# Optimization experiments

Measured on AMD Instinct MI355X. Metric: run time of the kernel, lower is better.

## Reference

```python
import jax, jax.numpy as jnp
import numpy as np

B, N, C, H, W = 8, 512, 3, 16, 16
K, P, E = 2, 4, 1           # K: hop levels == filter taps, P: attn heads, E: edge feature sets
SLOPE = 0.2                 # LeakyReLU slope in attention
GAT_DIMS = {'d0': (128, 128), 'd1': (512, 32), 'u0': (128, 64),
            'u1': (256, 128), 's0': (128, 128), 's1': (512, 64)}


def _conv(x, w, b):
    pad = w.shape[-1] // 2
    y = jax.lax.conv_general_dilated(x, w, (1, 1), [(pad, pad), (pad, pad)],
                                     dimension_numbers=('NCHW', 'OIHW', 'NCHW'))
    return y + b[None, :, None, None]


def _gat(x, S, wk, wq, wf, b):
    # x: (B,G,N); S: (B,E,N,N) binary GSO. KeyQuery attention + K-tap attentional filter.
    key = jnp.einsum('pegf,bgn->bpefn', wk, x)
    qry = jnp.einsum('pegf,bgn->bpefn', wq, x)
    # scores[...,n,m]: logit of node n attending to neighbor m
    scores = jax.nn.leaky_relu(jnp.einsum('bpefn,bpefm->bpenm', qry, key), SLOPE)
    mask = (jnp.abs(S) > 1e-9)[:, None]                    # (B,1,E,N,N)
    aij = jnp.where(mask, jax.nn.softmax(jnp.where(mask, scores, -1e9), axis=-1), 0.0)
    Pn, En, Kt, G, F = wf.shape
    xk = jnp.broadcast_to(x[:, None, None], (x.shape[0], Pn, En, G, x.shape[-1]))
    zs = [xk]
    for _ in range(Kt - 1):
        xk = jnp.einsum('bpegm,bpenm->bpegn', xk, aij)     # attention-weighted diffusion
        zs.append(xk)
    z = jnp.stack(zs, axis=3)                              # (B,P,E,K,G,N)
    y = jnp.einsum('bpekgn,pekgf->bpfn', z, wf) + b[None, None, :, None]
    y = jax.nn.relu(y)                                     # nonlinearity before head concat
    return y.reshape(y.shape[0], Pn * F, y.shape[-1])      # (B, P*F, N)


def _forward(x, Slist, conv0_w, conv0_b, conv1_w, conv1_b, flat_w, flat_b,
             d0_wk, d0_wq, d0_wf, d0_b, d1_wk, d1_wq, d1_wf, d1_b,
             u0_wk, u0_wq, u0_wf, u0_b, u1_wk, u1_wq, u1_wf, u1_b,
             s0_wk, s0_wq, s0_wf, s0_b, s1_wk, s1_wq, s1_wf, s1_b,
             dec0_w, dec0_b, dec1_w, dec1_b):
    Bn, Nn = x.shape[0], x.shape[1]
    h = x.reshape(Bn * Nn, C, H, W)
    e = jax.nn.relu(_conv(h, conv0_w, conv0_b))
    e = jax.nn.relu(_conv(e, conv1_w, conv1_b))
    e = e + h                                              # RES connection after encoder
    f = jax.nn.relu(e.reshape(Bn * Nn, -1) @ flat_w.T + flat_b)
    g = f.reshape(Bn, -1, Nn)                              # faithful torch reshape to (B, F, N)
    S0, S1 = Slist[:, 0:1], Slist[:, 1:2]
    p0 = g
    p1 = _gat(p0, S0, d0_wk, d0_wq, d0_wf, d0_b)           # downward pass
    p2 = _gat(p1, S1, d1_wk, d1_wq, d1_wf, d1_b)
    # upward pass + shortcuts (upward[l] uses S[K-l-1]; shortcut[K-1-l] on p[K-1-l])
    u0 = _gat(p2, S1, u0_wk, u0_wq, u0_wf, u0_b) + _gat(p1, S1, s1_wk, s1_wq, s1_wf, s1_b)
    u1 = _gat(u0, S0, u1_wk, u1_wq, u1_wf, u1_b) + _gat(p0, S0, s0_wk, s0_wq, s0_wf, s0_b)
    d = jax.nn.relu(u1.reshape(Bn * Nn, -1) @ dec0_w.T + dec0_b)
    out = jax.nn.softmax(d @ dec1_w.T + dec1_b, axis=-1)   # nn.Softmax() -> dim=1 on 2D input
    return out.reshape(Bn, Nn, -1)


def setup_inputs() -> dict:
    key = jax.random.key(0)
    ks = iter(jax.random.split(key, 64))
    def nrm(shape, s=0.1):
        return jax.random.normal(next(ks), shape, jnp.float32) * s
    x = jax.random.normal(next(ks), (B, N, C, H, W), jnp.float32)
    adj = (jax.random.uniform(next(ks), (B, K, N, N)) < 0.02).astype(jnp.float32)
    Slist = jnp.clip(adj + jnp.eye(N, dtype=jnp.float32)[None, None], 0.0, 1.0)
    inp = {'x': x, 'Slist': Slist,
           'conv0_w': nrm((32, C, 3, 3)), 'conv0_b': nrm((32,)),
           'conv1_w': nrm((C, 32, 3, 3)), 'conv1_b': nrm((C,)),
           'flat_w': nrm((128, C * H * W)), 'flat_b': nrm((128,))}
    for pre, (G, F) in GAT_DIMS.items():
        inp[pre + '_wk'] = nrm((P, E, G, F))
        inp[pre + '_wq'] = nrm((P, E, G, F))
        inp[pre + '_wf'] = nrm((P, E, K, G, F))
        inp[pre + '_b'] = nrm((F,))
    inp.update({'dec0_w': nrm((256, 512)), 'dec0_b': nrm((256,)),
                'dec1_w': nrm((5, 256)), 'dec1_b': nrm((5,))})
    return inp


def reference(x, Slist, conv0_w, conv0_b, conv1_w, conv1_b, flat_w, flat_b,
              d0_wk, d0_wq, d0_wf, d0_b, d1_wk, d1_wq, d1_wf, d1_b,
              u0_wk, u0_wq, u0_wf, u0_b, u1_wk, u1_wq, u1_wf, u1_b,
              s0_wk, s0_wq, s0_wf, s0_b, s1_wk, s1_wq, s1_wf, s1_b,
              dec0_w, dec0_b, dec1_w, dec1_b):
    return _forward(x, Slist, conv0_w, conv0_b, conv1_w, conv1_b, flat_w, flat_b,
                    d0_wk, d0_wq, d0_wf, d0_b, d1_wk, d1_wq, d1_wf, d1_b,
                    u0_wk, u0_wq, u0_wf, u0_b, u1_wk, u1_wq, u1_wf, u1_b,
                    s0_wk, s0_wq, s0_wf, s0_b, s1_wk, s1_wq, s1_wf, s1_b,
                    dec0_w, dec0_b, dec1_w, dec1_b)
```

## Files before the change

### kernel.cpp

```cpp
#include <hip/hip_runtime.h>
#include <hip/hip_bf16.h>
#include <math.h>

typedef unsigned short u16;
typedef unsigned int   u32;
typedef unsigned long long u64;

#define CAP 48

__device__ __forceinline__ float tof(u16 u){
  union { u32 i; float f; } v; v.i = ((u32)u) << 16; return v.f;
}
__device__ __forceinline__ u16 fromf(float f){
  union { float f; u32 i; } v; v.f = f;
  u32 x = v.i;
  return (u16)((x + 0x7fffu + ((x >> 16) & 1u)) >> 16);
}

__global__ void detect_dtype(const void* xp, int* flag){
  if(threadIdx.x == 0 && blockIdx.x == 0){
    const u16* p = (const u16*)xp;
    int outl = 0;
    for(int i = 0; i < 128; i++){
      u16 u = p[2*i];
      int e = (u >> 7) & 0xFF;
      if(u != 0 && (e < 100 || e > 140)) outl++;
    }
    *flag = (outl > 32) ? 1 : 0;
  }
}

struct WArgs {
  const void* p[34];
  int sz[34];
  int off[35];
};

__global__ __launch_bounds__(256) void convert_weights(WArgs wa, const int* flag,
                                                       float* __restrict__ arena, int total){
  int i = blockIdx.x * 256 + threadIdx.x;
  if(i >= total) return;
  int isf = *flag;
  int t = 0;
  while(wa.off[t+1] <= i) t++;
  int j = i - wa.off[t];
  float v = 0.f;
  if(j < wa.sz[t])
    v = isf ? ((const float*)wa.p[t])[j] : tof(((const u16*)wa.p[t])[j]);
  arena[i] = v;
}

__global__ __launch_bounds__(256) void transpose_w(const float* __restrict__ src,
                                                   float* __restrict__ dst, int R, int C){
  int i = blockIdx.x * 256 + threadIdx.x;
  if(i < R*C){
    int r = i / C, c = i - r*C;
    dst[(size_t)c*R + r] = src[i];
  }
}

__global__ __launch_bounds__(64) void build_nbr(const void* __restrict__ S,
                                                int* __restrict__ nbr_idx,
                                                int* __restrict__ nbr_cnt,
                                                const int* __restrict__ flag){
  int isf = *flag;
  int row  = blockIdx.x;
  int lane = threadIdx.x;
  int cnt = 0;
  for(int c = 0; c < 8; c++){
    int m = c*64 + lane;
    size_t idx = (size_t)row * 512 + m;
    float sv = isf ? ((const float*)S)[idx] : tof(((const u16*)S)[idx]);
    bool pred = fabsf(sv) > 1e-9f;
    unsigned long long mask = __ballot(pred);
    int pos = cnt + __popcll(mask & ((1ull << lane) - 1ull));
    if(pred && pos < CAP) nbr_idx[(size_t)row*CAP + pos] = m;
    cnt += __popcll(mask);
  }
  if(lane == 0) nbr_cnt[row] = cnt > CAP ? CAP : cnt;
}

__global__ __launch_bounds__(256) void encoder_conv(
    const void* __restrict__ x, const int* __restrict__ flag,
    const float* __restrict__ w0, const float* __restrict__ b0,
    const float* __restrict__ w1, const float* __restrict__ b1,
    float* __restrict__ e1n)
{
  __shared__ float xpad[3][18][18];
  __shared__ float e0p[16][18][18];

  int isf = *flag;
  int tid = threadIdx.x;
  size_t img = blockIdx.x;
  int py = tid >> 4, px = tid & 15;

  float* z1 = &xpad[0][0][0];
  for(int i = tid; i < 972; i += 256) z1[i] = 0.f;
  float* z2 = &e0p[0][0][0];
  for(int i = tid; i < 5184; i += 256) z2[i] = 0.f;
  __syncthreads();

  #pragma unroll
  for(int i = 0; i < 3; i++){
    size_t gi = img*768 + i*256 + tid;
    xpad[i][1+py][1+px] = isf ? ((const float*)x)[gi] : tof(((const u16*)x)[gi]);
  }
  __syncthreads();

  float acc1[3] = {0.f, 0.f, 0.f};

  for(int grp = 0; grp < 2; grp++){
    float acc0[16];
    #pragma unroll
    for(int o = 0; o < 16; o++) acc0[o] = 0.f;
    for(int i = 0; i < 3; i++){
      float rr[9];
      #pragma unroll
      for(int ky = 0; ky < 3; ky++)
        #pragma unroll
        for(int kx = 0; kx < 3; kx++)
          rr[ky*3+kx] = xpad[i][py+ky][px+kx];
      #pragma unroll
      for(int o = 0; o < 16; o++){
        #pragma unroll
        for(int t = 0; t < 9; t++)
          acc0[o] = fmaf(rr[t], w0[(grp*16+o)*27 + i*9 + t], acc0[o]);
      }
    }
    __syncthreads();
    #pragma unroll
    for(int o = 0; o < 16; o++)
      e0p[o][1+py][1+px] = fmaxf(acc0[o] + b0[grp*16 + o], 0.f);
    __syncthreads();

    for(int i = 0; i < 16; i++){
      float rr[9];
      #pragma unroll
      for(int ky = 0; ky < 3; ky++)
        #pragma unroll
        for(int kx = 0; kx < 3; kx++)
          rr[ky*3+kx] = e0p[i][py+ky][px+kx];
      int ic = grp*16 + i;
      #pragma unroll
      for(int o = 0; o < 3; o++){
        #pragma unroll
        for(int t = 0; t < 9; t++)
          acc1[o] = fmaf(rr[t], w1[o*288 + ic*9 + t], acc1[o]);
      }
    }
  }

  #pragma unroll
  for(int o = 0; o < 3; o++)
    e1n[img*768 + o*256 + tid] = fmaxf(acc1[o] + b1[o], 0.f) + xpad[o][1+py][1+px];
}

__global__ __launch_bounds__(256) void gemm_flat(
    const float* __restrict__ e1n, const float* __restrict__ fwT,
    const float* __restrict__ fb, float* __restrict__ g)
{
  __shared__ float As[16][68];
  __shared__ float Bs[16][68];
  int tid = threadIdx.x;
  int n0 = blockIdx.x * 64, m0 = blockIdx.y * 64;

  int lk = tid >> 4;
  int l4 = (tid & 15) * 4;
  int br = tid >> 2;
  int bc = (tid & 3) * 4;

  float acc[4][4];
  #pragma unroll
  for(int i = 0; i < 4; i++)
    #pragma unroll
    for(int jj = 0; jj < 4; jj++) acc[i][jj] = 0.f;

  int tm = tid >> 4, tn = tid & 15;
  for(int kt = 0; kt < 48; kt++){
    int k0 = kt*16;
    *(float4*)&As[lk][l4] = *(const float4*)&fwT[(size_t)(k0 + lk)*128 + m0 + l4];
    float4 bv = *(const float4*)&e1n[(size_t)(n0 + br)*768 + k0 + bc];
    Bs[bc+0][br] = bv.x; Bs[bc+1][br] = bv.y; Bs[bc+2][br] = bv.z; Bs[bc+3][br] = bv.w;
    __syncthreads();
    #pragma unroll
    for(int kk = 0; kk < 16; kk++){
      float4 a  = *(const float4*)&As[kk][tm*4];
      float4 xx = *(const float4*)&Bs[kk][tn*4];
      float av[4]  = {a.x, a.y, a.z, a.w};
      float xvv[4] = {xx.x, xx.y, xx.z, xx.w};
      #pragma unroll
      for(int i = 0; i < 4; i++)
        #pragma unroll
        for(int jj = 0; jj < 4; jj++)
          acc[i][jj] = fmaf(av[i], xvv[jj], acc[i][jj]);
    }
    __syncthreads();
  }

  #pragma unroll
  for(int jj = 0; jj < 4; jj++){
    int img = n0 + tn*4 + jj;
    float4 r = make_float4(fmaxf(acc[0][jj] + fb[m0+tm*4+0], 0.f),
                           fmaxf(acc[1][jj] + fb[m0+tm*4+1], 0.f),
                           fmaxf(acc[2][jj] + fb[m0+tm*4+2], 0.f),
                           fmaxf(acc[3][jj] + fb[m0+tm*4+3], 0.f));
    *(float4*)&g[(size_t)img*128 + m0 + tm*4] = r;
  }
}

struct KqP { const float* X; const float* wk; const float* wq; float* kqT;
             int G, F, my; };

__global__ __launch_bounds__(256) void gemm_kq2(KqP A, KqP B)
{
  __shared__ float Ws[32*68];
  __shared__ float Xs[32*68];
  int tid = threadIdx.x;
  int by = blockIdx.y;
  KqP P = (by < A.my) ? A : B;
  int lby = (by < A.my) ? by : (by - A.my);
  int bp = blockIdx.z;
  int b = bp >> 2, p = bp & 3;
  int n0 = blockIdx.x * 64, m0 = lby * 64;
  const float* Xb = P.X + (size_t)b * P.G * 512;

  int lk = tid >> 4;
  int l4 = (tid & 15) * 4;

  int mg = m0 + l4;
  int quad = mg / P.F;
  int mq = mg - quad * P.F;
  size_t GF = (size_t)P.G * P.F;
  const float* wb = (quad == 0 ? P.wk : P.wq) + (size_t)p * GF + mq;

  float acc[4][4];
  #pragma unroll
  for(int i = 0; i < 4; i++)
    #pragma unroll
    for(int jj = 0; jj < 4; jj++) acc[i][jj] = 0.f;

  int tm = tid >> 4, tn = tid & 15;
  int KT = P.G / 32;
  for(int kt = 0; kt < KT; kt++){
    int k = kt*32 + lk;
    *(float4*)&Ws[lk*68 + l4]      = *(const float4*)(wb + (size_t)k * P.F);
    *(float4*)&Ws[(lk+16)*68 + l4] = *(const float4*)(wb + (size_t)(k+16) * P.F);
    *(float4*)&Xs[lk*68 + l4]      = *(const float4*)(Xb + (size_t)k * 512 + n0 + l4);
    *(float4*)&Xs[(lk+16)*68 + l4] = *(const float4*)(Xb + (size_t)(k+16) * 512 + n0 + l4);
    __syncthreads();
    #pragma unroll
    for(int kk = 0; kk < 32; kk++){
      float4 a  = *(const float4*)&Ws[kk*68 + tm*4];
      float4 xx = *(const float4*)&Xs[kk*68 + tn*4];
      float av[4]  = {a.x, a.y, a.z, a.w};
      float xvv[4] = {xx.x, xx.y, xx.z, xx.w};
      #pragma unroll
      for(int i = 0; i < 4; i++)
        #pragma unroll
        for(int jj = 0; jj < 4; jj++)
          acc[i][jj] = fmaf(av[i], xvv[jj], acc[i][jj]);
    }
    __syncthreads();
  }

  int F2 = 2*P.F;
  float* ob = P.kqT + (size_t)bp * 512 * F2;
  #pragma unroll
  for(int jj = 0; jj < 4; jj++){
    float* orow = ob + (size_t)(n0 + tn*4 + jj) * F2 + m0 + tm*4;
    #pragma unroll
    for(int i = 0; i < 4; i++) orow[i] = acc[i][jj];
  }
}

struct AtP { const float* kqT; u64* ctrl; int F, s; };

__global__ __launch_bounds__(256) void attn2(
    AtP A, AtP B,
    const int* __restrict__ nbr_idx, const int* __restrict__ nbr_cnt)
{
  __shared__ float qs[16][132];
  __shared__ float sc[16][CAP];
  __shared__ float red[16][2];
  int tid = threadIdx.x;
  int n0 = blockIdx.x * 16;
  int bp = blockIdx.y;
  AtP P = (blockIdx.z == 0) ? A : B;
  int b = bp >> 2;
  int F = P.F;
  int F2 = 2*F;
  const float* kqT = P.kqT;

  int F4 = F >> 2;
  for(int i = tid; i < 16*F4; i += 256){
    int r = i / F4, c4 = (i - r*F4) * 4;
    *(float4*)&qs[r][c4] =
      *(const float4*)&kqT[((size_t)bp*512 + n0 + r)*F2 + F + c4];
  }
  __syncthreads();

  int r = tid >> 4;
  int t = tid & 15;
  int n = n0 + r;
  int srow = (b*2 + P.s)*512 + n;
  int cnt = nbr_cnt[srow];
  const int* il = nbr_idx + (size_t)srow * CAP;

  for(int j = t; j < cnt; j += 16){
    int m = il[j];
    const float* krow = kqT + ((size_t)bp*512 + m)*F2;
    float a = 0.f;
    for(int f = 0; f < F; f += 4){
      float4 k4 = *(const float4*)&krow[f];
      a = fmaf(qs[r][f],   k4.x, a);
      a = fmaf(qs[r][f+1], k4.y, a);
      a = fmaf(qs[r][f+2], k4.z, a);
      a = fmaf(qs[r][f+3], k4.w, a);
    }
    sc[r][j] = a >= 0.f ? a : 0.2f * a;
  }
  __syncthreads();

  if(t == 0){
    float mx = -1e30f;
    for(int j = 0; j < cnt; j++) mx = fmaxf(mx, sc[r][j]);
    float ssum = 0.f;
    for(int j = 0; j < cnt; j++) ssum += expf(sc[r][j] - mx);
    red[r][0] = mx; red[r][1] = ssum;
  }
  __syncthreads();

  float mx = red[r][0], ssum = red[r][1];
  u64* crow = P.ctrl + ((size_t)bp*512 + n)*CAP;
  for(int j = t; j < cnt; j += 16){
    float w = expf(sc[r][j] - mx) / ssum;
    crow[j] = (u64)__float_as_uint(w) | ((u64)(u32)il[j] << 32);
  }
}

struct FiP { const float* X; const u64* ctrl; float* Xp; int G, s, gy; };

__global__ __launch_bounds__(256) void fill_Xp4(
    FiP A, FiP B, const int* __restrict__ nbr_cnt)
{
  __shared__ float xi[512*18];

  int tid = threadIdx.x;
  int by = blockIdx.y;
  FiP P = (by < A.gy) ? A : B;
  int lby = (by < A.gy) ? by : (by - A.gy);
  int n0 = blockIdx.x * 64;
  int g0 = lby * 16;
  int bp = blockIdx.z;
  int b = bp >> 2;
  int srow0 = (b*2 + P.s)*512 + n0;

  const float* Xb = P.X + ((size_t)b * P.G + g0) * 512;
  for(int i = tid; i < 16*512; i += 256){
    int gl = i >> 9, m = i & 511;
    xi[m*18 + gl] = Xb[(size_t)gl*512 + m];
  }

  int n_l = tid & 63;
  int q   = tid >> 6;
  int cnt = nbr_cnt[srow0 + n_l];
  const u64* cn = P.ctrl + ((size_t)bp*512 + n0 + n_l)*CAP;
  __syncthreads();

  const float* xq = &xi[4*q];
  float a0=0.f, a1=0.f, a2=0.f, a3=0.f;
  for(int j0 = 0; j0 < cnt; j0 += 4){
    u64 c0 = cn[j0], c1 = cn[j0+1], c2 = cn[j0+2], c3 = cn[j0+3];
    int m0 = (int)(c0 >> 32) & 511;
    int m1 = (int)(c1 >> 32) & 511;
    int m2 = (int)(c2 >> 32) & 511;
    int m3 = (int)(c3 >> 32) & 511;
    float w0 = __uint_as_float((u32)c0);
    float w1 = (j0+1 < cnt) ? __uint_as_float((u32)c1) : 0.f;
    float w2 = (j0+2 < cnt) ? __uint_as_float((u32)c2) : 0.f;
    float w3 = (j0+3 < cnt) ? __uint_as_float((u32)c3) : 0.f;
    float2 g0a = *(const float2*)&xq[m0*18], g0b = *(const float2*)&xq[m0*18 + 2];
    float2 g1a = *(const float2*)&xq[m1*18], g1b = *(const float2*)&xq[m1*18 + 2];
    float2 g2a = *(const float2*)&xq[m2*18], g2b = *(const float2*)&xq[m2*18 + 2];
    float2 g3a = *(const float2*)&xq[m3*18], g3b = *(const float2*)&xq[m3*18 + 2];
    a0 = fmaf(w0, g0a.x, a0); a1 = fmaf(w0, g0a.y, a1);
    a2 = fmaf(w0, g0b.x, a2); a3 = fmaf(w0, g0b.y, a3);
    a0 = fmaf(w1, g1a.x, a0); a1 = fmaf(w1, g1a.y, a1);
    a2 = fmaf(w1, g1b.x, a2); a3 = fmaf(w1, g1b.y, a3);
    a0 = fmaf(w2, g2a.x, a0); a1 = fmaf(w2, g2a.y, a1);
    a2 = fmaf(w2, g2b.x, a2); a3 = fmaf(w2, g2b.y, a3);
    a0 = fmaf(w3, g3a.x, a0); a1 = fmaf(w3, g3a.y, a1);
    a2 = fmaf(w3, g3b.x, a2); a3 = fmaf(w3, g3b.y, a3);
  }

  float* ob = P.Xp + ((size_t)bp * P.G + g0 + 4*q) * 512 + n0 + n_l;
  ob[0]    = a0;
  ob[512]  = a1;
  ob[1024] = a2;
  ob[1536] = a3;
}

struct YP { const float* X; const float* Xp; const float* wf; const float* bias;
            float* out; int G, F, PF, acc, my; };

__global__ __launch_bounds__(256) void gemm_y2_32(YP A, YP B)
{
  __shared__ float Ws[32*68];
  __shared__ float Xs[32*68];
  int tid = threadIdx.x;
  int by = blockIdx.y;
  YP P = (by < A.my) ? A : B;
  int lby = (by < A.my) ? by : (by - A.my);
  int bp = blockIdx.z;
  int b = bp >> 2, p = bp & 3;
  int n0 = blockIdx.x * 64, m0 = lby * 64;
  int G = P.G, F = P.F;

  int lk = tid >> 4;
  int l4 = (tid & 15) * 4;
  int mg = m0 + l4;
  int fcl = mg < F ? mg : (F - 4);
  size_t GF2 = (size_t)2 * G * F;
  const float* wb = P.wf + (size_t)p * GF2 + fcl;

  float acc[4][4];
  #pragma unroll
  for(int i = 0; i < 4; i++)
    #pragma unroll
    for(int jj = 0; jj < 4; jj++) acc[i][jj] = 0.f;

  int tm = tid >> 4, tn = tid & 15;
  int KT = (2*G) / 32;
  for(int kt = 0; kt < KT; kt++){
    int c0 = kt*32 + lk;
    int c1 = c0 + 16;
    const float* xr0 = (c0 < G) ? (P.X  + ((size_t)b  * G + c0      ) * 512)
                                : (P.Xp + ((size_t)bp * G + (c0 - G)) * 512);
    const float* xr1 = (c1 < G) ? (P.X  + ((size_t)b  * G + c1      ) * 512)
                                : (P.Xp + ((size_t)bp * G + (c1 - G)) * 512);
    *(float4*)&Ws[lk*68 + l4]      = *(const float4*)(wb + (size_t)c0 * F);
    *(float4*)&Ws[(lk+16)*68 + l4] = *(const float4*)(wb + (size_t)c1 * F);
    *(float4*)&Xs[lk*68 + l4]      = *(const float4*)(xr0 + n0 + l4);
    *(float4*)&Xs[(lk+16)*68 + l4] = *(const float4*)(xr1 + n0 + l4);
    __syncthreads();
    #pragma unroll
    for(int kk = 0; kk < 32; kk++){
      float4 a  = *(const float4*)&Ws[kk*68 + tm*4];
      float4 xx = *(const float4*)&Xs[kk*68 + tn*4];
      float av[4]  = {a.x, a.y, a.z, a.w};
      float xvv[4] = {xx.x, xx.y, xx.z, xx.w};
      #pragma unroll
      for(int i = 0; i < 4; i++)
        #pragma unroll
        for(int jj = 0; jj < 4; jj++)
          acc[i][jj] = fmaf(av[i], xvv[jj], acc[i][jj]);
    }
    __syncthreads();
  }

  int mrow = m0 + tm*4;
  if(mrow < F){
    float* ob = P.out + ((size_t)b * P.PF + (size_t)p * F + mrow) * 512 + n0 + tn*4;
    #pragma unroll
    for(int i = 0; i < 4; i++){
      float bv = P.bias[mrow + i];
      float4 r = make_float4(fmaxf(acc[i][0] + bv, 0.f),
                             fmaxf(acc[i][1] + bv, 0.f),
                             fmaxf(acc[i][2] + bv, 0.f),
                             fmaxf(acc[i][3] + bv, 0.f));
      float* dst = ob + (size_t)i * 512;
      if(P.acc){
        float4 old = *(float4*)dst;
        r.x += old.x; r.y += old.y; r.z += old.z; r.w += old.w;
      }
      *(float4*)dst = r;
    }
  }
}

__global__ __launch_bounds__(256) void gemm_y2_K64(YP A, YP B)
{
  __shared__ float Ws[64*68];
  __shared__ float Xs[64*68];
  int tid = threadIdx.x;
  int by = blockIdx.y;
  YP P = (by < A.my) ? A : B;
  int lby = (by < A.my) ? by : (by - A.my);
  int bp = blockIdx.z;
  int b = bp >> 2, p = bp & 3;
  int n0 = blockIdx.x * 64, m0 = lby * 64;
  int G = P.G, F = P.F;

  int lk = tid >> 4;
  int l4 = (tid & 15) * 4;
  int mg = m0 + l4;
  int fcl = mg < F ? mg : (F - 4);
  size_t GF2 = (size_t)2 * G * F;
  const float* wb = P.wf + (size_t)p * GF2 + fcl;

  float acc[4][4];
  #pragma unroll
  for(int i = 0; i < 4; i++)
    #pragma unroll
    for(int jj = 0; jj < 4; jj++) acc[i][jj] = 0.f;

  int tm = tid >> 4, tn = tid & 15;
  int KT = (2*G) / 64;
  for(int kt = 0; kt < KT; kt++){
    #pragma unroll
    for(int kb = 0; kb < 4; kb++){
      int c = kt*64 + lk + kb*16;
      const float* xr = (c < G) ? (P.X  + ((size_t)b  * G + c      ) * 512)
                                : (P.Xp + ((size_t)bp * G + (c - G)) * 512);
      *(float4*)&Ws[(lk + kb*16)*68 + l4] = *(const float4*)(wb + (size_t)c * F);
      *(float4*)&Xs[(lk + kb*16)*68 + l4] = *(const float4*)(xr + n0 + l4);
    }
    __syncthreads();
    #pragma unroll
    for(int kk = 0; kk < 64; kk++){
      float4 a  = *(const float4*)&Ws[kk*68 + tm*4];
      float4 xx = *(const float4*)&Xs[kk*68 + tn*4];
      float av[4]  = {a.x, a.y, a.z, a.w};
      float xvv[4] = {xx.x, xx.y, xx.z, xx.w};
      #pragma unroll
      for(int i = 0; i < 4; i++)
        #pragma unroll
        for(int jj = 0; jj < 4; jj++)
          acc[i][jj] = fmaf(av[i], xvv[jj], acc[i][jj]);
    }
    __syncthreads();
  }

  int mrow = m0 + tm*4;
  if(mrow < F){
    float* ob = P.out + ((size_t)b * P.PF + (size_t)p * F + mrow) * 512 + n0 + tn*4;
    #pragma unroll
    for(int i = 0; i < 4; i++){
      float bv = P.bias[mrow + i];
      float4 r = make_float4(fmaxf(acc[i][0] + bv, 0.f),
                             fmaxf(acc[i][1] + bv, 0.f),
                             fmaxf(acc[i][2] + bv, 0.f),
                             fmaxf(acc[i][3] + bv, 0.f));
      float* dst = ob + (size_t)i * 512;
      if(P.acc){
        float4 old = *(float4*)dst;
        r.x += old.x; r.y += old.y; r.z += old.z; r.w += old.w;
      }
      *(float4*)dst = r;
    }
  }
}

__global__ __launch_bounds__(256) void add_vec(float* __restrict__ dst,
                                               const float* __restrict__ src, int n4){
  int i = blockIdx.x * 256 + threadIdx.x;
  if(i < n4){
    float4 a = ((const float4*)dst)[i];
    float4 b = ((const float4*)src)[i];
    a.x += b.x; a.y += b.y; a.z += b.z; a.w += b.w;
    ((float4*)dst)[i] = a;
  }
}

__global__ __launch_bounds__(256) void gemm_dec0(
    const float* __restrict__ u1, const float* __restrict__ w0T,
    const float* __restrict__ b0, float* __restrict__ d)
{
  __shared__ float As[16][68];
  __shared__ float Bs[16][68];
  int tid = threadIdx.x;
  int n0 = blockIdx.x * 64;
  int m0 = blockIdx.y * 64;

  int lk = tid >> 4;
  int l4 = (tid & 15) * 4;
  int br = tid >> 2;
  int bc = (tid & 3) * 4;

  float acc[4][4];
  #pragma unroll
  for(int i = 0; i < 4; i++)
    #pragma unroll
    for(int jj = 0; jj < 4; jj++) acc[i][jj] = 0.f;

  int tm = tid >> 4, tn = tid & 15;
  for(int kt = 0; kt < 32; kt++){
    int k0 = kt*16;
    *(float4*)&As[lk][l4] = *(const float4*)&w0T[(size_t)(k0 + lk)*256 + m0 + l4];
    float4 bv = *(const float4*)&u1[(size_t)(n0 + br)*512 + k0 + bc];
    Bs[bc+0][br] = bv.x; Bs[bc+1][br] = bv.y; Bs[bc+2][br] = bv.z; Bs[bc+3][br] = bv.w;
    __syncthreads();
    #pragma unroll
    for(int kk = 0; kk < 16; kk++){
      float4 a  = *(const float4*)&As[kk][tm*4];
      float4 xx = *(const float4*)&Bs[kk][tn*4];
      float av[4]  = {a.x, a.y, a.z, a.w};
      float xvv[4] = {xx.x, xx.y, xx.z, xx.w};
      #pragma unroll
      for(int i = 0; i < 4; i++)
        #pragma unroll
        for(int jj = 0; jj < 4; jj++)
          acc[i][jj] = fmaf(av[i], xvv[jj], acc[i][jj]);
    }
    __syncthreads();
  }

  #pragma unroll
  for(int jj = 0; jj < 4; jj++){
    int row = n0 + tn*4 + jj;
    float4 r = make_float4(fmaxf(acc[0][jj] + b0[m0+tm*4+0], 0.f),
                           fmaxf(acc[1][jj] + b0[m0+tm*4+1], 0.f),
                           fmaxf(acc[2][jj] + b0[m0+tm*4+2], 0.f),
                           fmaxf(acc[3][jj] + b0[m0+tm*4+3], 0.f));
    *(float4*)&d[(size_t)row*256 + m0 + tm*4] = r;
  }
}

__global__ __launch_bounds__(64) void decoder2(
    const float* __restrict__ d,
    const float* __restrict__ w1, const float* __restrict__ b1,
    const int* __restrict__ flag, void* __restrict__ outp)
{
  __shared__ float ds[256];
  __shared__ float lg[5];
  int r = blockIdx.x, lane = threadIdx.x;
  for(int i = lane; i < 256; i += 64) ds[i] = d[(size_t)r*256 + i];
  __syncthreads();

  if(lane < 5){
    float a = 0.f;
    const float* wr = w1 + (size_t)lane * 256;
    for(int i = 0; i < 256; i++) a = fmaf(ds[i], wr[i], a);
    lg[lane] = a + b1[lane];
  }
  __syncthreads();
  if(lane < 5){
    float mx = lg[0];
    for(int i = 1; i < 5; i++) mx = fmaxf(mx, lg[i]);
    float ssum = 0.f;
    for(int i = 0; i < 5; i++) ssum += expf(lg[i] - mx);
    float v = expf(lg[lane] - mx) / ssum;
    if(*flag) ((float*)outp)[(size_t)r*5 + lane] = v;
    else      ((u16*)outp)[(size_t)r*5 + lane] = fromf(v);
  }
}

extern "C" void kernel_launch(void* const* d_in, const int* in_sizes, int n_in,
                              void* d_out, int out_size, void* d_ws, size_t ws_size,
                              hipStream_t stream)
{
  (void)n_in; (void)out_size; (void)ws_size;
  const void* x = d_in[0];
  const void* S = d_in[1];

  float* wsf   = (float*)d_ws;
  int*   flag  = (int*)d_ws;
  float* arena = wsf + 1024;

  WArgs wa;
  long long aoff[35]; aoff[0] = 0;
  for(int t = 0; t < 34; t++){
    wa.p[t]  = d_in[2 + t];
    wa.sz[t] = in_sizes[2 + t];
    wa.off[t] = (int)aoff[t];
    aoff[t+1] = aoff[t] + ((in_sizes[2 + t] + 15) & ~15);
  }
  wa.off[34] = (int)aoff[34];
  int total = (int)aoff[34];

  size_t cur = 1024 + (size_t)((total + 1023) & ~1023);
  float* g    = wsf + cur; cur += 524288;
  float* p1   = wsf + cur; cur += 2097152;
  float* p2   = wsf + cur; cur += 524288;
  float* u0b  = wsf + cur; cur += 1048576;
  float* u0c  = wsf + cur; cur += 1048576;
  float* u1c  = wsf + cur; cur += 2097152;
  float* u1b  = p1;
  u64*   ctrlA= (u64*)(wsf + cur); cur += (size_t)32*512*CAP*2;
  u64*   ctrlB= (u64*)(wsf + cur); cur += (size_t)32*512*CAP*2;
  float* fwT  = wsf + cur; cur += 98304;
  float* dw0T = wsf + cur; cur += 131072;
  int*   ncnt = (int*)(wsf + cur); cur += 8192;
  int*   nidx = (int*)(wsf + cur); cur += (size_t)8192 * CAP;
  float* pool = wsf + cur; cur += 10485760;

  float* e1n   = pool;
  float* kqT0  = pool;
  float* Xp0   = pool;
  float* kqT1  = pool;
  float* kqT5  = pool + 4194304;
  float* Xp1   = pool;
  float* Xp5   = pool + 8388608;
  float* kqT2  = pool;
  float* kqT3  = pool + 2097152;
  float* Xp2   = pool;
  float* Xp3   = pool + 2097152;
  float* kqT4  = pool;
  float* Xp4   = pool;
  float* dbuf  = pool;

  const float* A[34];
  for(int t = 0; t < 34; t++) A[t] = arena + aoff[t];
  const float* c0w = A[0], *c0b = A[1], *c1w = A[2], *c1b = A[3];
  const float* fw  = A[4], *fb  = A[5];
  const float *wk_[6], *wq_[6], *wf_[6], *bias_[6];
  for(int l = 0; l < 6; l++){
    wk_[l]   = A[6 + 4*l];
    wq_[l]   = A[7 + 4*l];
    wf_[l]   = A[8 + 4*l];
    bias_[l] = A[9 + 4*l];
  }
  const float* dw0 = A[30], *db0 = A[31], *dw1 = A[32], *db1 = A[33];

  detect_dtype<<<1, 64, 0, stream>>>(x, flag);
  convert_weights<<<(total + 255)/256, 256, 0, stream>>>(wa, flag, arena, total);
  transpose_w<<<(98304 + 255)/256, 256, 0, stream>>>(fw, fwT, 128, 768);
  transpose_w<<<(131072 + 255)/256, 256, 0, stream>>>(dw0, dw0T, 256, 512);
  build_nbr<<<8192, 64, 0, stream>>>(S, nidx, ncnt, flag);
  encoder_conv<<<4096, 256, 0, stream>>>(x, flag, c0w, c0b, c1w, c1b, e1n);
  gemm_flat<<<dim3(64, 2), 256, 0, stream>>>(e1n, fwT, fb, g);

  {
    KqP k0 = { g, wk_[0], wq_[0], kqT0, 128, 128, 4 };
    gemm_kq2<<<dim3(8, 4, 32), 256, 0, stream>>>(k0, k0);
    AtP a0 = { kqT0, ctrlA, 128, 0 };
    attn2<<<dim3(32, 32, 1), 256, 0, stream>>>(a0, a0, nidx, ncnt);
    FiP f0 = { g, ctrlA, Xp0, 128, 0, 8 };
    fill_Xp4<<<dim3(8, 8, 32), 256, 0, stream>>>(f0, f0, ncnt);
    YP y0 = { g, Xp0, wf_[0], bias_[0], p1, 128, 128, 512, 0, 2 };
    gemm_y2_32<<<dim3(8, 2, 32), 256, 0, stream>>>(y0, y0);
  }

  {
    KqP k1 = { p1, wk_[1], wq_[1], kqT1, 512,  32, 1 };
    KqP k5 = { g,  wk_[4], wq_[4], kqT5, 128, 128, 4 };
    gemm_kq2<<<dim3(8, 5, 32), 256, 0, stream>>>(k1, k5);
    AtP a1 = { kqT1, ctrlA,  32, 1 };
    AtP a5 = { kqT5, ctrlB, 128, 0 };
    attn2<<<dim3(32, 32, 2), 256, 0, stream>>>(a1, a5, nidx, ncnt);
    FiP f1 = { p1, ctrlA, Xp1, 512, 1, 32 };
    FiP f5 = { g,  ctrlB, Xp5, 128, 0, 8 };
    fill_Xp4<<<dim3(8, 40, 32), 256, 0, stream>>>(f1, f5, ncnt);
    YP y1 = { p1, Xp1, wf_[1], bias_[1], p2,  512,  32, 128, 0, 1 };
    YP y5 = { g,  Xp5, wf_[4], bias_[4], u1c, 128, 128, 512, 0, 2 };
    gemm_y2_K64<<<dim3(8, 3, 32), 256, 0, stream>>>(y1, y5);
  }

  {
    KqP k2 = { p2, wk_[2], wq_[2], kqT2, 128, 64, 2 };
    KqP k3 = { p1, wk_[5], wq_[5], kqT3, 512, 64, 2 };
    gemm_kq2<<<dim3(8, 4, 32), 256, 0, stream>>>(k2, k3);
    AtP a2 = { kqT2, ctrlA, 64, 1 };
    AtP a3 = { kqT3, ctrlB, 64, 1 };
    attn2<<<dim3(32, 32, 2), 256, 0, stream>>>(a2, a3, nidx, ncnt);
    FiP f2 = { p2, ctrlA, Xp2, 128, 1, 8 };
    FiP f3 = { p1, ctrlB, Xp3, 512, 1, 32 };
    fill_Xp4<<<dim3(8, 40, 32), 256, 0, stream>>>(f2, f3, ncnt);
    YP y2 = { p2, Xp2, wf_[2], bias_[2], u0b, 128, 64, 256, 0, 1 };
    YP y3 = { p1, Xp3, wf_[5], bias_[5], u0c, 512, 64, 256, 0, 1 };
    gemm_y2_K64<<<dim3(8, 2, 32), 256, 0, stream>>>(y2, y3);
    add_vec<<<1024, 256, 0, stream>>>(u0b, u0c, 262144);
  }

  {
    KqP k4 = { u0b, wk_[3], wq_[3], kqT4, 256, 128, 4 };
    gemm_kq2<<<dim3(8, 4, 32), 256, 0, stream>>>(k4, k4);
    AtP a4 = { kqT4, ctrlA, 128, 0 };
    attn2<<<dim3(32, 32, 1), 256, 0, stream>>>(a4, a4, nidx, ncnt);
    FiP f4 = { u0b, ctrlA, Xp4, 256, 0, 16 };
    fill_Xp4<<<dim3(8, 16, 32), 256, 0, stream>>>(f4, f4, ncnt);
    YP y4 = { u0b, Xp4, wf_[3], bias_[3], u1b, 256, 128, 512, 0, 2 };
    gemm_y2_32<<<dim3(8, 2, 32), 256, 0, stream>>>(y4, y4);
    add_vec<<<2048, 256, 0, stream>>>(u1b, u1c, 524288);
  }

  gemm_dec0<<<dim3(64, 4), 256, 0, stream>>>(u1b, dw0T, db0, dbuf);
  decoder2<<<4096, 64, 0, stream>>>(dbuf, dw1, db1, flag, d_out);
}
```

Baseline: 875.5 us.

## Split-K the large-G key/query and filter GEMMs across extra blocks

The key/query GEMMs and the output filter GEMMs for the G=512 layers (d1, s1) are split along the reduction dimension into two halves. Each half runs as its own group of blocks in a new three-way combined launch, which adds parallelism and balances work against the smaller layers that share the launch. Partial sums go to scratch buffers and are merged by new sum2_vec and combine_y kernels, and combine_y also applies bias and ReLU. The cost is two extra launches per stage plus extra global memory traffic for the partials, and the scratch buffers alias pool, u0b and ctrlA regions.

```diff
diff --git a/kernel.cpp b/kernel.cpp
--- a/kernel.cpp
+++ b/kernel.cpp
@@ -209,16 +209,18 @@
 }
 
 struct KqP { const float* X; const float* wk; const float* wq; float* kqT;
-             int G, F, my; };
-
-__global__ __launch_bounds__(256) void gemm_kq2(KqP A, KqP B)
+             int G, F, my, k0, k1; };
+
+__global__ __launch_bounds__(256) void gemm_kq3(KqP A, KqP B, KqP C)
 {
   __shared__ float Ws[32*68];
   __shared__ float Xs[32*68];
   int tid = threadIdx.x;
   int by = blockIdx.y;
-  KqP P = (by < A.my) ? A : B;
-  int lby = (by < A.my) ? by : (by - A.my);
+  KqP P; int lby;
+  if(by < A.my){ P = A; lby = by; }
+  else if(by < A.my + B.my){ P = B; lby = by - A.my; }
+  else { P = C; lby = by - A.my - B.my; }
   int bp = blockIdx.z;
   int b = bp >> 2, p = bp & 3;
   int n0 = blockIdx.x * 64, m0 = lby * 64;
@@ -240,8 +242,8 @@
     for(int jj = 0; jj < 4; jj++) acc[i][jj] = 0.f;
 
   int tm = tid >> 4, tn = tid & 15;
-  int KT = P.G / 32;
-  for(int kt = 0; kt < KT; kt++){
+  int kt0 = P.k0 / 32, kt1 = P.k1 / 32;
+  for(int kt = kt0; kt < kt1; kt++){
     int k = kt*32 + lk;
     *(float4*)&Ws[lk*68 + l4]      = *(const float4*)(wb + (size_t)k * P.F);
     *(float4*)&Ws[(lk+16)*68 + l4] = *(const float4*)(wb + (size_t)(k+16) * P.F);
@@ -270,6 +272,17 @@
     float* orow = ob + (size_t)(n0 + tn*4 + jj) * F2 + m0 + tm*4;
     #pragma unroll
     for(int i = 0; i < 4; i++) orow[i] = acc[i][jj];
+  }
+}
+
+__global__ __launch_bounds__(256) void sum2_vec(float* __restrict__ out,
+                                                const float* __restrict__ a,
+                                                const float* __restrict__ b, int n4){
+  int i = blockIdx.x * 256 + threadIdx.x;
+  if(i < n4){
+    float4 x = ((const float4*)a)[i];
+    float4 y = ((const float4*)b)[i];
+    ((float4*)out)[i] = make_float4(x.x+y.x, x.y+y.y, x.z+y.z, x.w+y.w);
   }
 }
 
@@ -401,7 +414,108 @@
 }
 
 struct YP { const float* X; const float* Xp; const float* wf; const float* bias;
-            float* out; int G, F, PF, acc, my; };
+            float* out; int G, F, PF, acc, my, c0, c1, raw; };
+
+__global__ __launch_bounds__(256) void gemm_y3(YP A, YP B, YP C)
+{
+  __shared__ float Ws[64*68];
+  __shared__ float Xs[64*68];
+  int tid = threadIdx.x;
+  int by = blockIdx.y;
+  YP P; int lby;
+  if(by < A.my){ P = A; lby = by; }
+  else if(by < A.my + B.my){ P = B; lby = by - A.my; }
+  else { P = C; lby = by - A.my - B.my; }
+  int bp = blockIdx.z;
+  int b = bp >> 2, p = bp & 3;
+  int n0 = blockIdx.x * 64, m0 = lby * 64;
+  int G = P.G, F = P.F;
+
+  int lk = tid >> 4;
+  int l4 = (tid & 15) * 4;
+  int mg = m0 + l4;
+  int fcl = mg < F ? mg : (F - 4);
+  size_t GF2 = (size_t)2 * G * F;
+  const float* wb = P.wf + (size_t)p * GF2 + fcl;
+
+  float acc[4][4];
+  #pragma unroll
+  for(int i = 0; i < 4; i++)
+    #pragma unroll
+    for(int jj = 0; jj < 4; jj++) acc[i][jj] = 0.f;
+
+  int tm = tid >> 4, tn = tid & 15;
+  int kt0 = P.c0 / 64, kt1 = P.c1 / 64;
+  for(int kt = kt0; kt < kt1; kt++){
+    #pragma unroll
+    for(int kb = 0; kb < 4; kb++){
+      int c = kt*64 + lk + kb*16;
+      const float* xr = (c < G) ? (P.X  + ((size_t)b  * G + c      ) * 512)
+                                : (P.Xp + ((size_t)bp * G + (c - G)) * 512);
+      *(float4*)&Ws[(lk + kb*16)*68 + l4] = *(const float4*)(wb + (size_t)c * F);
+      *(float4*)&Xs[(lk + kb*16)*68 + l4] = *(const float4*)(xr + n0 + l4);
+    }
+    __syncthreads();
+    #pragma unroll
+    for(int kk = 0; kk < 64; kk++){
+      float4 a  = *(const float4*)&Ws[kk*68 + tm*4];
+      float4 xx = *(const float4*)&Xs[kk*68 + tn*4];
+      float av[4]  = {a.x, a.y, a.z, a.w};
+      float xvv[4] = {xx.x, xx.y, xx.z, xx.w};
+      #pragma unroll
+      for(int i = 0; i < 4; i++)
+        #pragma unroll
+        for(int jj = 0; jj < 4; jj++)
+          acc[i][jj] = fmaf(av[i], xvv[jj], acc[i][jj]);
+    }
+    __syncthreads();
+  }
+
+  int mrow = m0 + tm*4;
+  if(mrow < F){
+    float* ob = P.out + ((size_t)b * P.PF + (size_t)p * F + mrow) * 512 + n0 + tn*4;
+    if(P.raw){
+      #pragma unroll
+      for(int i = 0; i < 4; i++)
+        *(float4*)(ob + (size_t)i * 512) =
+          make_float4(acc[i][0], acc[i][1], acc[i][2], acc[i][3]);
+    } else {
+      #pragma unroll
+      for(int i = 0; i < 4; i++){
+        float bv = P.bias[mrow + i];
+        float4 r = make_float4(fmaxf(acc[i][0] + bv, 0.f),
+                               fmaxf(acc[i][1] + bv, 0.f),
+                               fmaxf(acc[i][2] + bv, 0.f),
+                               fmaxf(acc[i][3] + bv, 0.f));
+        float* dst = ob + (size_t)i * 512;
+        if(P.acc){
+          float4 old = *(float4*)dst;
+          r.x += old.x; r.y += old.y; r.z += old.z; r.w += old.w;
+        }
+        *(float4*)dst = r;
+      }
+    }
+  }
+}
+
+__global__ __launch_bounds__(256) void combine_y(
+    float* __restrict__ out, const float* __restrict__ s0,
+    const float* __restrict__ s1, const float* __restrict__ bias,
+    int F, int PF, int n4)
+{
+  int i = blockIdx.x * 256 + threadIdx.x;
+  if(i < n4){
+    int row = i >> 7;
+    int mrow = (row % PF) % F;
+    float bv = bias[mrow];
+    float4 a = ((const float4*)s0)[i];
+    float4 b = ((const float4*)s1)[i];
+    ((float4*)out)[i] = make_float4(fmaxf(a.x + b.x + bv, 0.f),
+                                    fmaxf(a.y + b.y + bv, 0.f),
+                                    fmaxf(a.z + b.z + bv, 0.f),
+                                    fmaxf(a.w + b.w + bv, 0.f));
+  }
+}
 
 __global__ __launch_bounds__(256) void gemm_y2_32(YP A, YP B)
 {
@@ -445,79 +559,6 @@
     __syncthreads();
     #pragma unroll
     for(int kk = 0; kk < 32; kk++){
-      float4 a  = *(const float4*)&Ws[kk*68 + tm*4];
-      float4 xx = *(const float4*)&Xs[kk*68 + tn*4];
-      float av[4]  = {a.x, a.y, a.z, a.w};
-      float xvv[4] = {xx.x, xx.y, xx.z, xx.w};
-      #pragma unroll
-      for(int i = 0; i < 4; i++)
-        #pragma unroll
-        for(int jj = 0; jj < 4; jj++)
-          acc[i][jj] = fmaf(av[i], xvv[jj], acc[i][jj]);
-    }
-    __syncthreads();
-  }
-
-  int mrow = m0 + tm*4;
-  if(mrow < F){
-    float* ob = P.out + ((size_t)b * P.PF + (size_t)p * F + mrow) * 512 + n0 + tn*4;
-    #pragma unroll
-    for(int i = 0; i < 4; i++){
-      float bv = P.bias[mrow + i];
-      float4 r = make_float4(fmaxf(acc[i][0] + bv, 0.f),
-                             fmaxf(acc[i][1] + bv, 0.f),
-                             fmaxf(acc[i][2] + bv, 0.f),
-                             fmaxf(acc[i][3] + bv, 0.f));
-      float* dst = ob + (size_t)i * 512;
-      if(P.acc){
-        float4 old = *(float4*)dst;
-        r.x += old.x; r.y += old.y; r.z += old.z; r.w += old.w;
-      }
-      *(float4*)dst = r;
-    }
-  }
-}
-
-__global__ __launch_bounds__(256) void gemm_y2_K64(YP A, YP B)
-{
-  __shared__ float Ws[64*68];
-  __shared__ float Xs[64*68];
-  int tid = threadIdx.x;
-  int by = blockIdx.y;
-  YP P = (by < A.my) ? A : B;
-  int lby = (by < A.my) ? by : (by - A.my);
-  int bp = blockIdx.z;
-  int b = bp >> 2, p = bp & 3;
-  int n0 = blockIdx.x * 64, m0 = lby * 64;
-  int G = P.G, F = P.F;
-
-  int lk = tid >> 4;
-  int l4 = (tid & 15) * 4;
-  int mg = m0 + l4;
-  int fcl = mg < F ? mg : (F - 4);
-  size_t GF2 = (size_t)2 * G * F;
-  const float* wb = P.wf + (size_t)p * GF2 + fcl;
-
-  float acc[4][4];
-  #pragma unroll
-  for(int i = 0; i < 4; i++)
-    #pragma unroll
-    for(int jj = 0; jj < 4; jj++) acc[i][jj] = 0.f;
-
-  int tm = tid >> 4, tn = tid & 15;
-  int KT = (2*G) / 64;
-  for(int kt = 0; kt < KT; kt++){
-    #pragma unroll
-    for(int kb = 0; kb < 4; kb++){
-      int c = kt*64 + lk + kb*16;
-      const float* xr = (c < G) ? (P.X  + ((size_t)b  * G + c      ) * 512)
-                                : (P.Xp + ((size_t)bp * G + (c - G)) * 512);
-      *(float4*)&Ws[(lk + kb*16)*68 + l4] = *(const float4*)(wb + (size_t)c * F);
-      *(float4*)&Xs[(lk + kb*16)*68 + l4] = *(const float4*)(xr + n0 + l4);
-    }
-    __syncthreads();
-    #pragma unroll
-    for(int kk = 0; kk < 64; kk++){
       float4 a  = *(const float4*)&Ws[kk*68 + tm*4];
       float4 xx = *(const float4*)&Xs[kk*68 + tn*4];
       float av[4]  = {a.x, a.y, a.z, a.w};
@@ -688,16 +729,25 @@
   float* kqT0  = pool;
   float* Xp0   = pool;
   float* kqT1  = pool;
+  float* pk1s0 = pool + 1048576;
+  float* pk1s1 = pool + 2097152;
   float* kqT5  = pool + 4194304;
   float* Xp1   = pool;
   float* Xp5   = pool + 8388608;
   float* kqT2  = pool;
   float* kqT3  = pool + 2097152;
+  float* pk3s0 = pool + 4194304;
+  float* pk3s1 = pool + 6291456;
   float* Xp2   = pool;
   float* Xp3   = pool + 2097152;
   float* kqT4  = pool;
   float* Xp4   = pool;
   float* dbuf  = pool;
+
+  float* yp1s0 = u0b;
+  float* yp1s1 = u0b + 524288;
+  float* yp3s0 = (float*)ctrlA;
+  float* yp3s1 = (float*)ctrlA + 1048576;
 
   const float* A[34];
   for(int t = 0; t < 34; t++) A[t] = arena + aoff[t];
@@ -721,55 +771,63 @@
   gemm_flat<<<dim3(64, 2), 256, 0, stream>>>(e1n, fwT, fb, g);
 
   {
-    KqP k0 = { g, wk_[0], wq_[0], kqT0, 128, 128, 4 };
-    gemm_kq2<<<dim3(8, 4, 32), 256, 0, stream>>>(k0, k0);
+    KqP k0 = { g, wk_[0], wq_[0], kqT0, 128, 128, 4, 0, 128 };
+    gemm_kq3<<<dim3(8, 4, 32), 256, 0, stream>>>(k0, k0, k0);
     AtP a0 = { kqT0, ctrlA, 128, 0 };
     attn2<<<dim3(32, 32, 1), 256, 0, stream>>>(a0, a0, nidx, ncnt);
     FiP f0 = { g, ctrlA, Xp0, 128, 0, 8 };
     fill_Xp4<<<dim3(8, 8, 32), 256, 0, stream>>>(f0, f0, ncnt);
-    YP y0 = { g, Xp0, wf_[0], bias_[0], p1, 128, 128, 512, 0, 2 };
+    YP y0 = { g, Xp0, wf_[0], bias_[0], p1, 128, 128, 512, 0, 2, 0, 256, 0 };
     gemm_y2_32<<<dim3(8, 2, 32), 256, 0, stream>>>(y0, y0);
   }
 
   {
-    KqP k1 = { p1, wk_[1], wq_[1], kqT1, 512,  32, 1 };
-    KqP k5 = { g,  wk_[4], wq_[4], kqT5, 128, 128, 4 };
-    gemm_kq2<<<dim3(8, 5, 32), 256, 0, stream>>>(k1, k5);
+    KqP k1a = { p1, wk_[1], wq_[1], pk1s0, 512,  32, 1,   0, 256 };
+    KqP k1b = { p1, wk_[1], wq_[1], pk1s1, 512,  32, 1, 256, 512 };
+    KqP k5  = { g,  wk_[4], wq_[4], kqT5,  128, 128, 4,   0, 128 };
+    gemm_kq3<<<dim3(8, 6, 32), 256, 0, stream>>>(k1a, k1b, k5);
+    sum2_vec<<<1024, 256, 0, stream>>>(kqT1, pk1s0, pk1s1, 262144);
     AtP a1 = { kqT1, ctrlA,  32, 1 };
     AtP a5 = { kqT5, ctrlB, 128, 0 };
     attn2<<<dim3(32, 32, 2), 256, 0, stream>>>(a1, a5, nidx, ncnt);
     FiP f1 = { p1, ctrlA, Xp1, 512, 1, 32 };
     FiP f5 = { g,  ctrlB, Xp5, 128, 0, 8 };
     fill_Xp4<<<dim3(8, 40, 32), 256, 0, stream>>>(f1, f5, ncnt);
-    YP y1 = { p1, Xp1, wf_[1], bias_[1], p2,  512,  32, 128, 0, 1 };
-    YP y5 = { g,  Xp5, wf_[4], bias_[4], u1c, 128, 128, 512, 0, 2 };
-    gemm_y2_K64<<<dim3(8, 3, 32), 256, 0, stream>>>(y1, y5);
+    YP y1a = { p1, Xp1, wf_[1], bias_[1], yp1s0, 512,  32, 128, 0, 1,   0,  512, 1 };
+    YP y1b = { p1, Xp1, wf_[1], bias_[1], yp1s1, 512,  32, 128, 0, 1, 512, 1024, 1 };
+    YP y5  = { g,  Xp5, wf_[4], bias_[4], u1c,   128, 128, 512, 0, 2,   0,  256, 0 };
+    gemm_y3<<<dim3(8, 4, 32), 256, 0, stream>>>(y1a, y1b, y5);
+    combine_y<<<512, 256, 0, stream>>>(p2, yp1s0, yp1s1, bias_[1], 32, 128, 131072);
   }
 
   {
-    KqP k2 = { p2, wk_[2], wq_[2], kqT2, 128, 64, 2 };
-    KqP k3 = { p1, wk_[5], wq_[5], kqT3, 512, 64, 2 };
-    gemm_kq2<<<dim3(8, 4, 32), 256, 0, stream>>>(k2, k3);
+    KqP k2  = { p2, wk_[2], wq_[2], kqT2,  128, 64, 2,   0, 128 };
+    KqP k3a = { p1, wk_[5], wq_[5], pk3s0, 512, 64, 2,   0, 256 };
+    KqP k3b = { p1, wk_[5], wq_[5], pk3s1, 512, 64, 2, 256, 512 };
+    gemm_kq3<<<dim3(8, 6, 32), 256, 0, stream>>>(k2, k3a, k3b);
+    sum2_vec<<<2048, 256, 0, stream>>>(kqT3, pk3s0, pk3s1, 524288);
     AtP a2 = { kqT2, ctrlA, 64, 1 };
     AtP a3 = { kqT3, ctrlB, 64, 1 };
     attn2<<<dim3(32, 32, 2), 256, 0, stream>>>(a2, a3, nidx, ncnt);
     FiP f2 = { p2, ctrlA, Xp2, 128, 1, 8 };
     FiP f3 = { p1, ctrlB, Xp3, 512, 1, 32 };
     fill_Xp4<<<dim3(8, 40, 32), 256, 0, stream>>>(f2, f3, ncnt);
-    YP y2 = { p2, Xp2, wf_[2], bias_[2], u0b, 128, 64, 256, 0, 1 };
-    YP y3 = { p1, Xp3, wf_[5], bias_[5], u0c, 512, 64, 256, 0, 1 };
-    gemm_y2_K64<<<dim3(8, 2, 32), 256, 0, stream>>>(y2, y3);
+    YP y2  = { p2, Xp2, wf_[2], bias_[2], u0b,   128, 64, 256, 0, 1,   0,  256, 0 };
+    YP y3a = { p1, Xp3, wf_[5], bias_[5], yp3s0, 512, 64, 256, 0, 1,   0,  512, 1 };
+    YP y3b = { p1, Xp3, wf_[5], bias_[5], yp3s1, 512, 64, 256, 0, 1, 512, 1024, 1 };
+    gemm_y3<<<dim3(8, 3, 32), 256, 0, stream>>>(y2, y3a, y3b);
+    combine_y<<<1024, 256, 0, stream>>>(u0c, yp3s0, yp3s1, bias_[5], 64, 256, 262144);
     add_vec<<<1024, 256, 0, stream>>>(u0b, u0c, 262144);
   }
 
   {
-    KqP k4 = { u0b, wk_[3], wq_[3], kqT4, 256, 128, 4 };
-    gemm_kq2<<<dim3(8, 4, 32), 256, 0, stream>>>(k4, k4);
+    KqP k4 = { u0b, wk_[3], wq_[3], kqT4, 256, 128, 4, 0, 256 };
+    gemm_kq3<<<dim3(8, 4, 32), 256, 0, stream>>>(k4, k4, k4);
     AtP a4 = { kqT4, ctrlA, 128, 0 };
     attn2<<<dim3(32, 32, 1), 256, 0, stream>>>(a4, a4, nidx, ncnt);
     FiP f4 = { u0b, ctrlA, Xp4, 256, 0, 16 };
     fill_Xp4<<<dim3(8, 16, 32), 256, 0, stream>>>(f4, f4, ncnt);
-    YP y4 = { u0b, Xp4, wf_[3], bias_[3], u1b, 256, 128, 512, 0, 2 };
+    YP y4 = { u0b, Xp4, wf_[3], bias_[3], u1b, 256, 128, 512, 0, 2, 0, 512, 0 };
     gemm_y2_32<<<dim3(8, 2, 32), 256, 0, stream>>>(y4, y4);
     add_vec<<<2048, 256, 0, stream>>>(u1b, u1c, 524288);
   }
```

New measurement: 863.6 us. About the same (-1.4%).
